# Performance work log

Hardware: AMD Instinct MI355X
Metric: run time of the kernel (lower is better)

Reference implementation:

```python
import jax, jax.numpy as jnp
import numpy as np

B, S, IN, E, H, NH = 32, 1024, 16, 128, 256, 4
DH = E // NH
EPS = 1e-5


def _ln(x, g, b):
    mu = jnp.mean(x, axis=-1, keepdims=True)
    var = jnp.mean(jnp.square(x - mu), axis=-1, keepdims=True)
    return (x - mu) * jax.lax.rsqrt(var + EPS) * g + b


def setup_inputs() -> dict:
    key = jax.random.key(0)
    ks = iter(jax.random.split(key, 32))
    n = lambda shape, s=0.02: jax.random.normal(next(ks), shape, jnp.float32) * s
    inp = {
        "x": jax.random.normal(next(ks), (B, S, IN), jnp.float32),
        "mask": jax.random.uniform(next(ks), (B, S), jnp.float32),
        "embed_w": n((E, IN)), "embed_b": jnp.zeros((E,), jnp.float32),
        # 3 encoder layers, params stacked on leading layer axis
        "in_proj_w": n((3, 3 * E, E)), "in_proj_b": jnp.zeros((3, 3 * E), jnp.float32),
        "out_w": n((3, E, E)), "out_b": jnp.zeros((3, E), jnp.float32),
        "ln1_g": jnp.ones((3, E), jnp.float32), "ln1_b": jnp.zeros((3, E), jnp.float32),
        "ln2_g": jnp.ones((3, E), jnp.float32), "ln2_b": jnp.zeros((3, E), jnp.float32),
        "ffn_w1": n((3, E, E)), "ffn_b1": jnp.zeros((3, E), jnp.float32),
        "ffn_w2": n((3, E, E)), "ffn_b2": jnp.zeros((3, E), jnp.float32),
        "cls_w1": n((H, E)), "cls_b1": jnp.zeros((H,), jnp.float32),
        "cls_w2": n((H, H)), "cls_b2": jnp.zeros((H,), jnp.float32),
        "cls_w3": n((H, H)), "cls_b3": jnp.zeros((H,), jnp.float32),
        "cls_w4": n((1, H)), "cls_b4": jnp.zeros((1,), jnp.float32),
    }
    return inp


def _encoder_layer(x, ipw, ipb, ow, ob, g1, b1, g2, b2, w1, fb1, w2, fb2):
    # PyTorch TransformerEncoderLayer, norm_first=False (post-norm), relu FFN
    qkv = x @ ipw.T + ipb                      # [B,S,3E]
    q, k, v = jnp.split(qkv, 3, axis=-1)
    q = q.reshape(B, S, NH, DH).transpose(0, 2, 1, 3)
    k = k.reshape(B, S, NH, DH).transpose(0, 2, 1, 3)
    v = v.reshape(B, S, NH, DH).transpose(0, 2, 1, 3)
    scores = jnp.einsum("bhqd,bhkd->bhqk", q, k) / np.sqrt(DH)  # naive O(S^2) math SDPA
    attn = jax.nn.softmax(scores, axis=-1)
    o = jnp.einsum("bhqk,bhkd->bhqd", attn, v)
    o = o.transpose(0, 2, 1, 3).reshape(B, S, E) @ ow.T + ob
    x = _ln(x + o, g1, b1)
    ff = jax.nn.relu(x @ w1.T + fb1) @ w2.T + fb2
    return _ln(x + ff, g2, b2)


def reference(x, mask, embed_w, embed_b, in_proj_w, in_proj_b, out_w, out_b,
              ln1_g, ln1_b, ln2_g, ln2_b, ffn_w1, ffn_b1, ffn_w2, ffn_b2,
              cls_w1, cls_b1, cls_w2, cls_b2, cls_w3, cls_b3, cls_w4, cls_b4):
    h = jax.nn.relu(x @ embed_w.T + embed_b)   # [B,S,E]
    for i in range(3):
        h = _encoder_layer(h, in_proj_w[i], in_proj_b[i], out_w[i], out_b[i],
                           ln1_g[i], ln1_b[i], ln2_g[i], ln2_b[i],
                           ffn_w1[i], ffn_b1[i], ffn_w2[i], ffn_b2[i])
    pooled = jnp.sum(h * mask[:, :, None], axis=1)  # [B,E] masked sum pool
    z = jax.nn.relu(pooled @ cls_w1.T + cls_b1)
    z = jax.nn.relu(z @ cls_w2.T + cls_b2)
    z = jax.nn.relu(z @ cls_w3.T + cls_b3)
    return jax.nn.sigmoid(z @ cls_w4.T + cls_b4)    # [B,1]
```

## Files before the change

kernel.cpp:

```cpp
#include <hip/hip_runtime.h>
#include <hip/hip_bf16.h>
#include <math.h>

#define B 32
#define S 1024
#define IN_DIM 16
#define E 128
#define NH 4
#define DH 32
#define HDIM 256
#define ROWS (B*S)
#define EPS 1e-5f

#define N_IPW (3*384*128)
#define N_SQ  (3*128*128)
#define NCVT ((N_IPW + 3*N_SQ) / 256)

typedef __bf16 bf16x8 __attribute__((ext_vector_type(8)));
typedef __bf16 bf16x4 __attribute__((ext_vector_type(4)));
typedef __bf16 bf16x2 __attribute__((ext_vector_type(2)));
typedef float f32x4 __attribute__((ext_vector_type(4)));
typedef float f32x16 __attribute__((ext_vector_type(16)));

#define MFMA16 __builtin_amdgcn_mfma_f32_16x16x32_bf16
#define MFMA32 __builtin_amdgcn_mfma_f32_32x32x16_bf16

union BF2U { bf16x2 b; unsigned int u; };
__device__ inline unsigned int pk2(float a, float b) {
    BF2U x; x.b[0] = (__bf16)a; x.b[1] = (__bf16)b; return x.u;
}

union U8 { bf16x8 v8; bf16x4 v4[2]; unsigned u4[4]; };
__device__ inline void st8(__bf16* p, bf16x8 v) {
    U8 u; u.v8 = v;
    *(bf16x4*)p = u.v4[0];
    *(bf16x4*)(p + 4) = u.v4[1];
}
__device__ inline bf16x8 ld8(const __bf16* p) {
    U8 u;
    u.v4[0] = *(const bf16x4*)p;
    u.v4[1] = *(const bf16x4*)(p + 4);
    return u.v8;
}

__global__ __launch_bounds__(256) void k_embedcvt(
        const float* __restrict__ ipw, const float* __restrict__ ow,
        const float* __restrict__ w1, const float* __restrict__ w2,
        __bf16* __restrict__ wbo,
        const float* __restrict__ x, const float* __restrict__ W,
        const float* __restrict__ bias, __bf16* __restrict__ hb)
{
    int t = threadIdx.x;
    if (blockIdx.x < NCVT) {
        int i = blockIdx.x * 256 + t;
        float v;
        if (i < N_IPW) v = ipw[i];
        else if (i < N_IPW + N_SQ) v = ow[i - N_IPW];
        else if (i < N_IPW + 2 * N_SQ) v = w1[i - N_IPW - N_SQ];
        else v = w2[i - N_IPW - 2 * N_SQ];
        wbo[i] = (__bf16)v;
        return;
    }
    int row0 = (blockIdx.x - NCVT) * 16;
    __shared__ float xs[16][16];
    xs[t >> 4][t & 15] = x[(row0 + (t >> 4)) * IN_DIM + (t & 15)];
    __syncthreads();
    int sub = t >> 7, tc = t & 127;
    float w[16];
#pragma unroll
    for (int i = 0; i < 16; ++i) w[i] = W[tc * 16 + i];
    float bb = bias[tc];
#pragma unroll
    for (int rr = 0; rr < 8; ++rr) {
        int lr = sub * 8 + rr;
        float acc = bb;
#pragma unroll
        for (int i = 0; i < 16; ++i) acc += xs[lr][i] * w[i];
        hb[(size_t)(row0 + lr) * E + tc] = (__bf16)fmaxf(acc, 0.f);
    }
}

__global__ __launch_bounds__(1024, 4) void k_qkvattn(
        const __bf16* __restrict__ hb, const __bf16* __restrict__ Wip,
        const float* __restrict__ bip, __bf16* __restrict__ O)
{
    __shared__ __attribute__((aligned(16))) __bf16 Ksh[1024][36];
    __shared__ __attribute__((aligned(16))) __bf16 Vsh[32][1036];
    __shared__ float lscr[16][32];

    int t = threadIdx.x, lane = t & 63, wv = t >> 6;
    int l15 = lane & 15, quad = lane >> 4;
    int l31 = lane & 31, hi = lane >> 5;
    int lb = ((blockIdx.x & 7) << 5) | (blockIdx.x >> 3);
    int half = lb & 1, bh = lb >> 1;
    int hh = bh & 3, b = bh >> 2;

    const __bf16* hpanel = hb + (size_t)b * S * E;

    const float qscale = 0.1767766952966369f * 1.4426950408889634f * 8388608.0f;
    const float C2 = 1065101558.0f;
    f32x16 cinit16, z16;
#pragma unroll
    for (int i = 0; i < 16; ++i) { cinit16[i] = C2; z16[i] = 0.f; }

    bf16x8 bQ[2];
    {
        bf16x8 bWq[8];
#pragma unroll
        for (int ch = 0; ch < 8; ++ch)
            bWq[ch] = *(const bf16x8*)&Wip[(size_t)(hh*32 + l31)*128 + ch*16 + hi*8];
        float bq = bip[hh*32 + l31];
        int qrow0 = half*512 + wv*32;
        f32x16 aq = z16;
#pragma unroll
        for (int ch = 0; ch < 8; ++ch) {
            bf16x8 ah = *(const bf16x8*)&hpanel[(size_t)(qrow0 + l31)*128 + ch*16 + hi*8];
            aq = MFMA32(ah, bWq[ch], aq, 0, 0, 0);
        }
        __bf16* PmS = &Ksh[wv*32][0];
#pragma unroll
        for (int r = 0; r < 16; ++r) {
            int q = (r & 3) + 8*(r >> 2) + 4*hi;
            PmS[q*36 + l31] = (__bf16)((aq[r] + bq) * qscale);
        }
        __asm__ __volatile__("" ::: "memory");
        bQ[0] = ld8(&PmS[l31*36 + hi*8]);
        bQ[1] = ld8(&PmS[l31*36 + 16 + hi*8]);
        __asm__ __volatile__("" ::: "memory");
    }
    __syncthreads();

    {
        bf16x8 bWk[2][4], bWv[2][4];
#pragma unroll
        for (int df = 0; df < 2; ++df)
#pragma unroll
            for (int kc = 0; kc < 4; ++kc) {
                bWk[df][kc] = *(const bf16x8*)&Wip[(size_t)(128 + hh*32 + df*16 + l15)*128 + kc*32 + quad*8];
                bWv[df][kc] = *(const bf16x8*)&Wip[(size_t)(256 + hh*32 + df*16 + l15)*128 + kc*32 + quad*8];
            }
        float bk0 = bip[128 + hh*32 + l15],  bk1 = bip[128 + hh*32 + 16 + l15];
        float bvb0 = bip[256 + hh*32 + l15], bvb1 = bip[256 + hh*32 + 16 + l15];
        int srow = wv*16 + l15;
        bf16x8 af[4], ag[4];
#pragma unroll
        for (int kc = 0; kc < 4; ++kc)
            af[kc] = *(const bf16x8*)&hpanel[(size_t)srow*128 + kc*32 + quad*8];
        const f32x4 z4 = {0.f, 0.f, 0.f, 0.f};
        for (int c = 0; c < 4; ++c) {
            if (c < 3) {
#pragma unroll
                for (int kc = 0; kc < 4; ++kc)
                    ag[kc] = *(const bf16x8*)&hpanel[(size_t)((c+1)*256 + srow)*128 + kc*32 + quad*8];
            }
            f32x4 k0 = z4, k1 = z4, v0 = z4, v1 = z4;
#pragma unroll
            for (int kc = 0; kc < 4; ++kc) {
                k0 = MFMA16(af[kc], bWk[0][kc], k0, 0, 0, 0);
                k1 = MFMA16(af[kc], bWk[1][kc], k1, 0, 0, 0);
                v0 = MFMA16(af[kc], bWv[0][kc], v0, 0, 0, 0);
                v1 = MFMA16(af[kc], bWv[1][kc], v1, 0, 0, 0);
            }
            int s0 = c*256 + wv*16 + quad*4;
#pragma unroll
            for (int r = 0; r < 4; ++r) {
                Ksh[s0 + r][l15]      = (__bf16)(k0[r] + bk0);
                Ksh[s0 + r][16 + l15] = (__bf16)(k1[r] + bk1);
            }
            uint2 u0, u1;
            u0.x = pk2(v0[0] + bvb0, v0[1] + bvb0);
            u0.y = pk2(v0[2] + bvb0, v0[3] + bvb0);
            u1.x = pk2(v1[0] + bvb1, v1[1] + bvb1);
            u1.y = pk2(v1[2] + bvb1, v1[3] + bvb1);
            *(uint2*)&Vsh[l15][s0] = u0;
            *(uint2*)&Vsh[16 + l15][s0] = u1;
#pragma unroll
            for (int kc = 0; kc < 4; ++kc) af[kc] = ag[kc];
        }
    }
    __syncthreads();

    f32x16 o = z16;
    float lsum = 0.f;

    for (int c = 0; c < 16; ++c) {
        bf16x8 aK[2][2];
#pragma unroll
        for (int sub = 0; sub < 2; ++sub)
#pragma unroll
            for (int dh = 0; dh < 2; ++dh)
                aK[sub][dh] = ld8(&Ksh[c*64 + sub*32 + l31][dh*16 + hi*8]);
        bf16x8 bVf[4];
#pragma unroll
        for (int ch = 0; ch < 4; ++ch) {
            U8 u;
            const __bf16* vp = &Vsh[l31][c*64 + ch*16 + hi*4];
            u.v4[0] = *(const bf16x4*)vp;
            u.v4[1] = *(const bf16x4*)(vp + 8);
            bVf[ch] = u.v8;
        }
#pragma unroll
        for (int sub = 0; sub < 2; ++sub) {
            f32x16 acc = cinit16;
            acc = MFMA32(aK[sub][0], bQ[0], acc, 0, 0, 0);
            acc = MFMA32(aK[sub][1], bQ[1], acc, 0, 0, 0);
#pragma unroll
            for (int g = 0; g < 2; ++g) {
                U8 u;
#pragma unroll
                for (int r = 0; r < 4; ++r) {
                    int ia = (int)acc[g*8 + 2*r];
                    int ib = (int)acc[g*8 + 2*r + 1];
                    u.u4[r] = __builtin_amdgcn_perm((unsigned)ib, (unsigned)ia, 0x07060302u);
                    lsum += __int_as_float(ia) + __int_as_float(ib);
                }
                o = MFMA32(u.v8, bVf[sub*2 + g], o, 0, 0, 0);
            }
        }
    }

    lsum += __shfl_xor(lsum, 32);
    float linv = 1.f / lsum;
    if (hi == 0) lscr[wv][l31] = linv;
    __asm__ __volatile__("" ::: "memory");
#pragma unroll
    for (int r = 0; r < 16; ++r) {
        int q = (r & 3) + 8*(r >> 2) + 4*hi;
        float li = lscr[wv][q];
        int row = half*512 + wv*32 + q;
        O[((size_t)(b * S) + row) * E + hh*32 + l31] = (__bf16)(o[r] * li);
    }
}

__global__ __launch_bounds__(512, 4) void k_layer2(const __bf16* __restrict__ t0b,
        const __bf16* __restrict__ Wo, const float* __restrict__ ob,
        const float* __restrict__ g1, const float* __restrict__ bt1,
        const __bf16* __restrict__ W1, const float* __restrict__ b1v,
        const __bf16* __restrict__ W2, const float* __restrict__ b2v,
        const float* __restrict__ g2, const float* __restrict__ bt2,
        __bf16* __restrict__ hb)
{
    __shared__ __attribute__((aligned(16))) __bf16 As[64][132];
    __shared__ __attribute__((aligned(16))) __bf16 Ws[128][132];
    __shared__ float red[2][64][2];
    int t = threadIdx.x;
    int m0 = blockIdx.x * 64;
    int arow = t >> 3, acol = (t & 7) * 16;
    int wrow = t >> 2, wcol = (t & 3) * 32;
    {
        const __bf16* Ap = t0b + (size_t)(m0 + arow) * 128 + acol;
#pragma unroll
        for (int j = 0; j < 2; ++j)
            st8(&As[arow][acol + j * 8], *(const bf16x8*)&Ap[j * 8]);
        const __bf16* Wp = Wo + (size_t)wrow * 128 + wcol;
#pragma unroll
        for (int j = 0; j < 4; ++j)
            st8(&Ws[wrow][wcol + j * 8], *(const bf16x8*)&Wp[j * 8]);
    }
    __syncthreads();
    int lane = t & 63, wv = t >> 6;
    int l15 = lane & 15, quad = lane >> 4;
    int nh = wv & 1, mh = wv >> 1;
    f32x4 acc[4];

#pragma unroll
    for (int i = 0; i < 4; ++i) acc[i] = (f32x4){0.f, 0.f, 0.f, 0.f};
#pragma unroll
    for (int kc = 0; kc < 4; ++kc) {
        bf16x8 aw[4], ba;
#pragma unroll
        for (int nc = 0; nc < 4; ++nc)
            aw[nc] = ld8(&Ws[nh * 64 + nc * 16 + l15][kc * 32 + quad * 8]);
        ba = ld8(&As[mh * 16 + l15][kc * 32 + quad * 8]);
#pragma unroll
        for (int nc = 0; nc < 4; ++nc)
            acc[nc] = MFMA16(aw[nc], ba, acc[nc], 0, 0, 0);
    }
    float s1 = 0.f, s2 = 0.f;
    int m = m0 + mh * 16 + l15;
#pragma unroll
    for (int nc = 0; nc < 4; ++nc) {
        float4 bv = *(const float4*)&ob[nh * 64 + nc * 16 + quad * 4];
        bf16x4 rv = *(const bf16x4*)&hb[(size_t)m * 128 + nh * 64 + nc * 16 + quad * 4];
        acc[nc][0] += bv.x + (float)rv[0];
        acc[nc][1] += bv.y + (float)rv[1];
        acc[nc][2] += bv.z + (float)rv[2];
        acc[nc][3] += bv.w + (float)rv[3];
#pragma unroll
        for (int i = 0; i < 4; ++i) {
            s1 += acc[nc][i];
            s2 += acc[nc][i] * acc[nc][i];
        }
    }
    s1 += __shfl_xor(s1, 16); s1 += __shfl_xor(s1, 32);
    s2 += __shfl_xor(s2, 16); s2 += __shfl_xor(s2, 32);
    if (quad == 0) {
        red[nh][mh * 16 + l15][0] = s1;
        red[nh][mh * 16 + l15][1] = s2;
    }
    __syncthreads();
    float mu, rs;
    {
        int r = mh * 16 + l15;
        float S1 = red[0][r][0] + red[1][r][0];
        float S2 = red[0][r][1] + red[1][r][1];
        mu = S1 * (1.f / 128.f);
        float var = S2 * (1.f / 128.f) - mu * mu;
        rs = rsqrtf(var + EPS);
    }
    bf16x4 res2[4];
#pragma unroll
    for (int nc = 0; nc < 4; ++nc) {
        float4 gv = *(const float4*)&g1[nh * 64 + nc * 16 + quad * 4];
        float4 bb = *(const float4*)&bt1[nh * 64 + nc * 16 + quad * 4];
        float o0 = (acc[nc][0] - mu) * rs * gv.x + bb.x;
        float o1 = (acc[nc][1] - mu) * rs * gv.y + bb.y;
        float o2 = (acc[nc][2] - mu) * rs * gv.z + bb.z;
        float o3 = (acc[nc][3] - mu) * rs * gv.w + bb.w;
        bf16x4 xb;
        xb[0] = (__bf16)o0; xb[1] = (__bf16)o1;
        xb[2] = (__bf16)o2; xb[3] = (__bf16)o3;
        res2[nc] = xb;
        *(bf16x4*)&As[mh * 16 + l15][nh * 64 + nc * 16 + quad * 4] = xb;
    }
    {
        const __bf16* Wp = W1 + (size_t)wrow * 128 + wcol;
#pragma unroll
        for (int j = 0; j < 4; ++j)
            st8(&Ws[wrow][wcol + j * 8], *(const bf16x8*)&Wp[j * 8]);
    }
    __syncthreads();

#pragma unroll
    for (int i = 0; i < 4; ++i) acc[i] = (f32x4){0.f, 0.f, 0.f, 0.f};
#pragma unroll
    for (int kc = 0; kc < 4; ++kc) {
        bf16x8 aw[4], ba;
#pragma unroll
        for (int nc = 0; nc < 4; ++nc)
            aw[nc] = ld8(&Ws[nh * 64 + nc * 16 + l15][kc * 32 + quad * 8]);
        ba = ld8(&As[mh * 16 + l15][kc * 32 + quad * 8]);
#pragma unroll
        for (int nc = 0; nc < 4; ++nc)
            acc[nc] = MFMA16(aw[nc], ba, acc[nc], 0, 0, 0);
    }
    __syncthreads();
#pragma unroll
    for (int nc = 0; nc < 4; ++nc) {
        float4 bv = *(const float4*)&b1v[nh * 64 + nc * 16 + quad * 4];
        float v0 = fmaxf(acc[nc][0] + bv.x, 0.f);
        float v1 = fmaxf(acc[nc][1] + bv.y, 0.f);
        float v2 = fmaxf(acc[nc][2] + bv.z, 0.f);
        float v3 = fmaxf(acc[nc][3] + bv.w, 0.f);
        uint2 u; u.x = pk2(v0, v1); u.y = pk2(v2, v3);
        *(uint2*)&As[mh * 16 + l15][nh * 64 + nc * 16 + quad * 4] = u;
    }
    {
        const __bf16* Wp = W2 + (size_t)wrow * 128 + wcol;
#pragma unroll
        for (int j = 0; j < 4; ++j)
            st8(&Ws[wrow][wcol + j * 8], *(const bf16x8*)&Wp[j * 8]);
    }
    __syncthreads();

#pragma unroll
    for (int i = 0; i < 4; ++i) acc[i] = (f32x4){0.f, 0.f, 0.f, 0.f};
#pragma unroll
    for (int kc = 0; kc < 4; ++kc) {
        bf16x8 aw[4], ba;
#pragma unroll
        for (int nc = 0; nc < 4; ++nc)
            aw[nc] = ld8(&Ws[nh * 64 + nc * 16 + l15][kc * 32 + quad * 8]);
        ba = ld8(&As[mh * 16 + l15][kc * 32 + quad * 8]);
#pragma unroll
        for (int nc = 0; nc < 4; ++nc)
            acc[nc] = MFMA16(aw[nc], ba, acc[nc], 0, 0, 0);
    }
    s1 = 0.f; s2 = 0.f;
#pragma unroll
    for (int nc = 0; nc < 4; ++nc) {
        float4 bv = *(const float4*)&b2v[nh * 64 + nc * 16 + quad * 4];
        acc[nc][0] += bv.x + (float)res2[nc][0];
        acc[nc][1] += bv.y + (float)res2[nc][1];
        acc[nc][2] += bv.z + (float)res2[nc][2];
        acc[nc][3] += bv.w + (float)res2[nc][3];
#pragma unroll
        for (int i = 0; i < 4; ++i) {
            s1 += acc[nc][i];
            s2 += acc[nc][i] * acc[nc][i];
        }
    }
    s1 += __shfl_xor(s1, 16); s1 += __shfl_xor(s1, 32);
    s2 += __shfl_xor(s2, 16); s2 += __shfl_xor(s2, 32);
    if (quad == 0) {
        red[nh][mh * 16 + l15][0] = s1;
        red[nh][mh * 16 + l15][1] = s2;
    }
    __syncthreads();
    {
        int r = mh * 16 + l15;
        float S1 = red[0][r][0] + red[1][r][0];
        float S2 = red[0][r][1] + red[1][r][1];
        mu = S1 * (1.f / 128.f);
        float var = S2 * (1.f / 128.f) - mu * mu;
        rs = rsqrtf(var + EPS);
    }
#pragma unroll
    for (int nc = 0; nc < 4; ++nc) {
        float4 gv = *(const float4*)&g2[nh * 64 + nc * 16 + quad * 4];
        float4 bb = *(const float4*)&bt2[nh * 64 + nc * 16 + quad * 4];
        float o0 = (acc[nc][0] - mu) * rs * gv.x + bb.x;
        float o1 = (acc[nc][1] - mu) * rs * gv.y + bb.y;
        float o2 = (acc[nc][2] - mu) * rs * gv.z + bb.z;
        float o3 = (acc[nc][3] - mu) * rs * gv.w + bb.w;
        uint2 u; u.x = pk2(o0, o1); u.y = pk2(o2, o3);
        *(uint2*)&hb[(size_t)m * 128 + nh * 64 + nc * 16 + quad * 4] = u;
    }
}

__global__ __launch_bounds__(256) void k_pool1(const __bf16* __restrict__ h,
        const float* __restrict__ mask, float* __restrict__ part)
{
    int bx = blockIdx.x;
    int b = bx >> 3, ch = bx & 7, t = threadIdx.x;
    int sg = t >> 4, cg = t & 15;
    __shared__ float red[16][128];
    float acc[8];
#pragma unroll
    for (int j = 0; j < 8; ++j) acc[j] = 0.f;
    const __bf16* hp = h + ((size_t)(b * S + ch * 128 + sg)) * E + cg * 8;
    const float* mp = mask + b * S + ch * 128 + sg;
#pragma unroll
    for (int k = 0; k < 8; ++k) {
        float m = mp[k * 16];
        bf16x8 hv = *(const bf16x8*)&hp[(size_t)(k * 16) * E];
#pragma unroll
        for (int j = 0; j < 8; ++j) acc[j] += (float)hv[j] * m;
    }
#pragma unroll
    for (int j = 0; j < 8; ++j) red[sg][cg * 8 + j] = acc[j];
    __syncthreads();
    if (t < 128) {
        float a = 0.f;
#pragma unroll
        for (int sgi = 0; sgi < 16; ++sgi) a += red[sgi][t];
        part[(size_t)bx * E + t] = a;
    }
}

__global__ __launch_bounds__(256) void k_head(const float* __restrict__ part,
        const float* __restrict__ cw1, const float* __restrict__ cb1,
        const float* __restrict__ cw2, const float* __restrict__ cb2,
        const float* __restrict__ cw3, const float* __restrict__ cb3,
        const float* __restrict__ cw4, const float* __restrict__ cb4,
        float* __restrict__ out)
{
    int b = blockIdx.x, t = threadIdx.x;
    __shared__ float p[128], za[256], zb[256];
    __shared__ float red4[4];
    if (t < 128) {
        float a = 0.f;
#pragma unroll
        for (int c = 0; c < 8; ++c) a += part[(size_t)(b * 8 + c) * 128 + t];
        p[t] = a;
    }
    __syncthreads();
    float a1 = cb1[t];
    for (int k = 0; k < 128; ++k) a1 += p[k] * cw1[t * 128 + k];
    za[t] = fmaxf(a1, 0.f);
    __syncthreads();
    float a2 = cb2[t];
    for (int k = 0; k < 256; ++k) a2 += za[k] * cw2[t * 256 + k];
    zb[t] = fmaxf(a2, 0.f);
    __syncthreads();
    float a3 = cb3[t];
    for (int k = 0; k < 256; ++k) a3 += zb[k] * cw3[t * 256 + k];
    float z3 = fmaxf(a3, 0.f);
    float prt = z3 * cw4[t];
#pragma unroll
    for (int o2 = 32; o2; o2 >>= 1) prt += __shfl_xor(prt, o2);
    if ((t & 63) == 0) red4[t >> 6] = prt;
    __syncthreads();
    if (t == 0) {
        float sum = red4[0] + red4[1] + red4[2] + red4[3] + cb4[0];
        out[b] = 1.f / (1.f + __expf(-sum));
    }
}

extern "C" void kernel_launch(void* const* d_in, const int* in_sizes, int n_in,
                              void* d_out, int out_size, void* d_ws, size_t ws_size,
                              hipStream_t stream)
{
    const float* x     = (const float*)d_in[0];
    const float* mask  = (const float*)d_in[1];
    const float* emb_w = (const float*)d_in[2];
    const float* emb_b = (const float*)d_in[3];
    const float* ipw   = (const float*)d_in[4];
    const float* ipb   = (const float*)d_in[5];
    const float* ow    = (const float*)d_in[6];
    const float* ob    = (const float*)d_in[7];
    const float* ln1g  = (const float*)d_in[8];
    const float* ln1b  = (const float*)d_in[9];
    const float* ln2g  = (const float*)d_in[10];
    const float* ln2b  = (const float*)d_in[11];
    const float* w1    = (const float*)d_in[12];
    const float* fb1   = (const float*)d_in[13];
    const float* w2    = (const float*)d_in[14];
    const float* fb2   = (const float*)d_in[15];
    const float* cw1   = (const float*)d_in[16];
    const float* cb1   = (const float*)d_in[17];
    const float* cw2   = (const float*)d_in[18];
    const float* cb2   = (const float*)d_in[19];
    const float* cw3   = (const float*)d_in[20];
    const float* cb3   = (const float*)d_in[21];
    const float* cw4   = (const float*)d_in[22];
    const float* cb4   = (const float*)d_in[23];

    char* p = (char*)d_ws;
    __bf16* hb   = (__bf16*)p;   p += (size_t)ROWS * E * 2;
    p += (size_t)ROWS * 256 * 2;
    p += (size_t)ROWS * 32 * 4 * 2 / 4;
    __bf16* t0b  = (__bf16*)p;   p += (size_t)ROWS * E * 2;
    __bf16* wb   = (__bf16*)p;   p += (size_t)(N_IPW + 3 * N_SQ) * 2;
    float* part  = (float*)p;    p += (size_t)B * 8 * E * 4;

    __bf16* wb_ipw = wb;
    __bf16* wb_ow  = wb + N_IPW;
    __bf16* wb_w1  = wb_ow + N_SQ;
    __bf16* wb_w2  = wb_w1 + N_SQ;

    k_embedcvt<<<NCVT + ROWS / 16, 256, 0, stream>>>(
        ipw, ow, w1, w2, wb, x, emb_w, emb_b, hb);
    for (int L = 0; L < 3; ++L) {
        k_qkvattn<<<B * NH * 2, 1024, 0, stream>>>(
            hb, wb_ipw + (size_t)L * 384 * 128, ipb + L * 384, t0b);
        k_layer2<<<ROWS / 64, 512, 0, stream>>>(
            t0b, wb_ow + (size_t)L * 128 * 128, ob + L * 128,
            ln1g + L * E, ln1b + L * E,
            wb_w1 + (size_t)L * 128 * 128, fb1 + L * 128,
            wb_w2 + (size_t)L * 128 * 128, fb2 + L * 128,
            ln2g + L * E, ln2b + L * E, hb);
    }
    k_pool1<<<B * 8, 256, 0, stream>>>(hb, mask, part);
    k_head<<<B, 256, 0, stream>>>(part, cw1, cb1, cw2, cb2, cw3, cb3, cw4, cb4,
                                  (float*)d_out);
}
```

Baseline: 306.5 us.

## Give each attention wave two query tiles, software-pipeline K/V loads, prefetch layer2 weights

The attention kernel now runs with 512 threads per block, and each wave handles two 32-row query tiles. Each K/V fragment loaded from shared memory is reused across both tiles, and the next chunk's K/V fragments are loaded while the current chunk computes. The layer2 kernel issues its global loads for the residual and the W1/W2 weights early into registers, so that global latency overlaps compute; its launch-bounds occupancy hint drops to 3. This trades higher register pressure and fewer waves per block for less LDS traffic and less exposed latency.

```diff
diff --git a/kernel.cpp b/kernel.cpp
--- a/kernel.cpp
+++ b/kernel.cpp
@@ -80,13 +80,13 @@
     }
 }
 
-__global__ __launch_bounds__(1024, 4) void k_qkvattn(
+__global__ __launch_bounds__(512, 2) void k_qkvattn(
         const __bf16* __restrict__ hb, const __bf16* __restrict__ Wip,
         const float* __restrict__ bip, __bf16* __restrict__ O)
 {
     __shared__ __attribute__((aligned(16))) __bf16 Ksh[1024][36];
     __shared__ __attribute__((aligned(16))) __bf16 Vsh[32][1036];
-    __shared__ float lscr[16][32];
+    __shared__ float lscr[8][64];
 
     int t = threadIdx.x, lane = t & 63, wv = t >> 6;
     int l15 = lane & 15, quad = lane >> 4;
@@ -103,29 +103,36 @@
 #pragma unroll
     for (int i = 0; i < 16; ++i) { cinit16[i] = C2; z16[i] = 0.f; }
 
-    bf16x8 bQ[2];
+    bf16x8 bQ[2][2];
     {
         bf16x8 bWq[8];
 #pragma unroll
         for (int ch = 0; ch < 8; ++ch)
             bWq[ch] = *(const bf16x8*)&Wip[(size_t)(hh*32 + l31)*128 + ch*16 + hi*8];
         float bq = bip[hh*32 + l31];
-        int qrow0 = half*512 + wv*32;
-        f32x16 aq = z16;
-#pragma unroll
-        for (int ch = 0; ch < 8; ++ch) {
-            bf16x8 ah = *(const bf16x8*)&hpanel[(size_t)(qrow0 + l31)*128 + ch*16 + hi*8];
-            aq = MFMA32(ah, bWq[ch], aq, 0, 0, 0);
-        }
-        __bf16* PmS = &Ksh[wv*32][0];
-#pragma unroll
-        for (int r = 0; r < 16; ++r) {
-            int q = (r & 3) + 8*(r >> 2) + 4*hi;
-            PmS[q*36 + l31] = (__bf16)((aq[r] + bq) * qscale);
+#pragma unroll
+        for (int qt = 0; qt < 2; ++qt) {
+            int qrow0 = half*512 + wv*64 + qt*32;
+            f32x16 aq = z16;
+#pragma unroll
+            for (int ch = 0; ch < 8; ++ch) {
+                bf16x8 ah = *(const bf16x8*)&hpanel[(size_t)(qrow0 + l31)*128 + ch*16 + hi*8];
+                aq = MFMA32(ah, bWq[ch], aq, 0, 0, 0);
+            }
+            __bf16* PmS = &Ksh[wv*128 + qt*32][0];
+#pragma unroll
+            for (int r = 0; r < 16; ++r) {
+                int q = (r & 3) + 8*(r >> 2) + 4*hi;
+                PmS[q*36 + l31] = (__bf16)((aq[r] + bq) * qscale);
+            }
         }
         __asm__ __volatile__("" ::: "memory");
-        bQ[0] = ld8(&PmS[l31*36 + hi*8]);
-        bQ[1] = ld8(&PmS[l31*36 + 16 + hi*8]);
+#pragma unroll
+        for (int qt = 0; qt < 2; ++qt) {
+            const __bf16* PmS = &Ksh[wv*128 + qt*32][0];
+            bQ[qt][0] = ld8(&PmS[l31*36 + hi*8]);
+            bQ[qt][1] = ld8(&PmS[l31*36 + 16 + hi*8]);
+        }
         __asm__ __volatile__("" ::: "memory");
     }
     __syncthreads();
@@ -147,11 +154,11 @@
         for (int kc = 0; kc < 4; ++kc)
             af[kc] = *(const bf16x8*)&hpanel[(size_t)srow*128 + kc*32 + quad*8];
         const f32x4 z4 = {0.f, 0.f, 0.f, 0.f};
-        for (int c = 0; c < 4; ++c) {
-            if (c < 3) {
+        for (int c = 0; c < 8; ++c) {
+            if (c < 7) {
 #pragma unroll
                 for (int kc = 0; kc < 4; ++kc)
-                    ag[kc] = *(const bf16x8*)&hpanel[(size_t)((c+1)*256 + srow)*128 + kc*32 + quad*8];
+                    ag[kc] = *(const bf16x8*)&hpanel[(size_t)((c+1)*128 + srow)*128 + kc*32 + quad*8];
             }
             f32x4 k0 = z4, k1 = z4, v0 = z4, v1 = z4;
 #pragma unroll
@@ -161,7 +168,7 @@
                 v0 = MFMA16(af[kc], bWv[0][kc], v0, 0, 0, 0);
                 v1 = MFMA16(af[kc], bWv[1][kc], v1, 0, 0, 0);
             }
-            int s0 = c*256 + wv*16 + quad*4;
+            int s0 = c*128 + wv*16 + quad*4;
 #pragma unroll
             for (int r = 0; r < 4; ++r) {
                 Ksh[s0 + r][l15]      = (__bf16)(k0[r] + bk0);
@@ -180,59 +187,94 @@
     }
     __syncthreads();
 
-    f32x16 o = z16;
-    float lsum = 0.f;
+    f32x16 o[2];
+    o[0] = z16; o[1] = z16;
+    float lsum[2] = {0.f, 0.f};
+
+    bf16x8 aK[2][2], bVf[4];
+#pragma unroll
+    for (int sub = 0; sub < 2; ++sub)
+#pragma unroll
+        for (int dh = 0; dh < 2; ++dh)
+            aK[sub][dh] = ld8(&Ksh[sub*32 + l31][dh*16 + hi*8]);
+#pragma unroll
+    for (int ch = 0; ch < 4; ++ch) {
+        U8 u;
+        const __bf16* vp = &Vsh[l31][ch*16 + hi*4];
+        u.v4[0] = *(const bf16x4*)vp;
+        u.v4[1] = *(const bf16x4*)(vp + 8);
+        bVf[ch] = u.v8;
+    }
 
     for (int c = 0; c < 16; ++c) {
-        bf16x8 aK[2][2];
-#pragma unroll
-        for (int sub = 0; sub < 2; ++sub)
-#pragma unroll
-            for (int dh = 0; dh < 2; ++dh)
-                aK[sub][dh] = ld8(&Ksh[c*64 + sub*32 + l31][dh*16 + hi*8]);
-        bf16x8 bVf[4];
-#pragma unroll
-        for (int ch = 0; ch < 4; ++ch) {
-            U8 u;
-            const __bf16* vp = &Vsh[l31][c*64 + ch*16 + hi*4];
-            u.v4[0] = *(const bf16x4*)vp;
-            u.v4[1] = *(const bf16x4*)(vp + 8);
-            bVf[ch] = u.v8;
-        }
-#pragma unroll
-        for (int sub = 0; sub < 2; ++sub) {
-            f32x16 acc = cinit16;
-            acc = MFMA32(aK[sub][0], bQ[0], acc, 0, 0, 0);
-            acc = MFMA32(aK[sub][1], bQ[1], acc, 0, 0, 0);
-#pragma unroll
-            for (int g = 0; g < 2; ++g) {
+        bf16x8 aKn[2][2], bVn[4];
+        if (c < 15) {
+#pragma unroll
+            for (int sub = 0; sub < 2; ++sub)
+#pragma unroll
+                for (int dh = 0; dh < 2; ++dh)
+                    aKn[sub][dh] = ld8(&Ksh[(c+1)*64 + sub*32 + l31][dh*16 + hi*8]);
+#pragma unroll
+            for (int ch = 0; ch < 4; ++ch) {
                 U8 u;
-#pragma unroll
-                for (int r = 0; r < 4; ++r) {
-                    int ia = (int)acc[g*8 + 2*r];
-                    int ib = (int)acc[g*8 + 2*r + 1];
-                    u.u4[r] = __builtin_amdgcn_perm((unsigned)ib, (unsigned)ia, 0x07060302u);
-                    lsum += __int_as_float(ia) + __int_as_float(ib);
+                const __bf16* vp = &Vsh[l31][(c+1)*64 + ch*16 + hi*4];
+                u.v4[0] = *(const bf16x4*)vp;
+                u.v4[1] = *(const bf16x4*)(vp + 8);
+                bVn[ch] = u.v8;
+            }
+        }
+#pragma unroll
+        for (int qt = 0; qt < 2; ++qt) {
+#pragma unroll
+            for (int sub = 0; sub < 2; ++sub) {
+                f32x16 acc = cinit16;
+                acc = MFMA32(aK[sub][0], bQ[qt][0], acc, 0, 0, 0);
+                acc = MFMA32(aK[sub][1], bQ[qt][1], acc, 0, 0, 0);
+#pragma unroll
+                for (int g = 0; g < 2; ++g) {
+                    U8 u;
+                    float ls = 0.f;
+#pragma unroll
+                    for (int r = 0; r < 4; ++r) {
+                        int ia = (int)acc[g*8 + 2*r];
+                        int ib = (int)acc[g*8 + 2*r + 1];
+                        u.u4[r] = __builtin_amdgcn_perm((unsigned)ib, (unsigned)ia, 0x07060302u);
+                        ls += __int_as_float(ia) + __int_as_float(ib);
+                    }
+                    lsum[qt] += ls;
+                    o[qt] = MFMA32(u.v8, bVf[sub*2 + g], o[qt], 0, 0, 0);
                 }
-                o = MFMA32(u.v8, bVf[sub*2 + g], o, 0, 0, 0);
-            }
-        }
-    }
-
-    lsum += __shfl_xor(lsum, 32);
-    float linv = 1.f / lsum;
-    if (hi == 0) lscr[wv][l31] = linv;
+            }
+        }
+        if (c < 15) {
+#pragma unroll
+            for (int sub = 0; sub < 2; ++sub)
+#pragma unroll
+                for (int dh = 0; dh < 2; ++dh)
+                    aK[sub][dh] = aKn[sub][dh];
+#pragma unroll
+            for (int ch = 0; ch < 4; ++ch) bVf[ch] = bVn[ch];
+        }
+    }
+
+#pragma unroll
+    for (int qt = 0; qt < 2; ++qt) {
+        float ls = lsum[qt] + __shfl_xor(lsum[qt], 32);
+        if (hi == 0) lscr[wv][qt*32 + l31] = 1.f / ls;
+    }
     __asm__ __volatile__("" ::: "memory");
 #pragma unroll
-    for (int r = 0; r < 16; ++r) {
-        int q = (r & 3) + 8*(r >> 2) + 4*hi;
-        float li = lscr[wv][q];
-        int row = half*512 + wv*32 + q;
-        O[((size_t)(b * S) + row) * E + hh*32 + l31] = (__bf16)(o[r] * li);
-    }
-}
-
-__global__ __launch_bounds__(512, 4) void k_layer2(const __bf16* __restrict__ t0b,
+    for (int qt = 0; qt < 2; ++qt)
+#pragma unroll
+        for (int r = 0; r < 16; ++r) {
+            int q = (r & 3) + 8*(r >> 2) + 4*hi;
+            float li = lscr[wv][qt*32 + q];
+            int row = half*512 + wv*64 + qt*32 + q;
+            O[((size_t)(b * S) + row) * E + hh*32 + l31] = (__bf16)(o[qt][r] * li);
+        }
+}
+
+__global__ __launch_bounds__(512, 3) void k_layer2(const __bf16* __restrict__ t0b,
         const __bf16* __restrict__ Wo, const float* __restrict__ ob,
         const float* __restrict__ g1, const float* __restrict__ bt1,
         const __bf16* __restrict__ W1, const float* __restrict__ b1v,
@@ -245,22 +287,36 @@
     __shared__ float red[2][64][2];
     int t = threadIdx.x;
     int m0 = blockIdx.x * 64;
-    int arow = t >> 3, acol = (t & 7) * 16;
-    int wrow = t >> 2, wcol = (t & 3) * 32;
-    {
-        const __bf16* Ap = t0b + (size_t)(m0 + arow) * 128 + acol;
-#pragma unroll
-        for (int j = 0; j < 2; ++j)
-            st8(&As[arow][acol + j * 8], *(const bf16x8*)&Ap[j * 8]);
-        const __bf16* Wp = Wo + (size_t)wrow * 128 + wcol;
-#pragma unroll
-        for (int j = 0; j < 4; ++j)
-            st8(&Ws[wrow][wcol + j * 8], *(const bf16x8*)&Wp[j * 8]);
-    }
-    __syncthreads();
     int lane = t & 63, wv = t >> 6;
     int l15 = lane & 15, quad = lane >> 4;
     int nh = wv & 1, mh = wv >> 1;
+    int m = m0 + mh * 16 + l15;
+    int arow = t >> 3, acol = (t & 7) * 16;
+    int wrow = t >> 2, wcol = (t & 3) * 32;
+
+    bf16x8 avr[2], w0r[4], w1r[4];
+    {
+        const __bf16* Ap = t0b + (size_t)(m0 + arow) * 128 + acol;
+        avr[0] = *(const bf16x8*)&Ap[0];
+        avr[1] = *(const bf16x8*)&Ap[8];
+        const __bf16* Wp0 = Wo + (size_t)wrow * 128 + wcol;
+        const __bf16* Wp1 = W1 + (size_t)wrow * 128 + wcol;
+#pragma unroll
+        for (int j = 0; j < 4; ++j) w0r[j] = *(const bf16x8*)&Wp0[j * 8];
+#pragma unroll
+        for (int j = 0; j < 4; ++j) w1r[j] = *(const bf16x8*)&Wp1[j * 8];
+    }
+    bf16x4 rv[4];
+#pragma unroll
+    for (int nc = 0; nc < 4; ++nc)
+        rv[nc] = *(const bf16x4*)&hb[(size_t)m * 128 + nh * 64 + nc * 16 + quad * 4];
+
+#pragma unroll
+    for (int j = 0; j < 2; ++j) st8(&As[arow][acol + j * 8], avr[j]);
+#pragma unroll
+    for (int j = 0; j < 4; ++j) st8(&Ws[wrow][wcol + j * 8], w0r[j]);
+    __syncthreads();
+
     f32x4 acc[4];
 
 #pragma unroll
@@ -277,15 +333,13 @@
             acc[nc] = MFMA16(aw[nc], ba, acc[nc], 0, 0, 0);
     }
     float s1 = 0.f, s2 = 0.f;
-    int m = m0 + mh * 16 + l15;
 #pragma unroll
     for (int nc = 0; nc < 4; ++nc) {
         float4 bv = *(const float4*)&ob[nh * 64 + nc * 16 + quad * 4];
-        bf16x4 rv = *(const bf16x4*)&hb[(size_t)m * 128 + nh * 64 + nc * 16 + quad * 4];
-        acc[nc][0] += bv.x + (float)rv[0];
-        acc[nc][1] += bv.y + (float)rv[1];
-        acc[nc][2] += bv.z + (float)rv[2];
-        acc[nc][3] += bv.w + (float)rv[3];
+        acc[nc][0] += bv.x + (float)rv[nc][0];
+        acc[nc][1] += bv.y + (float)rv[nc][1];
+        acc[nc][2] += bv.z + (float)rv[nc][2];
+        acc[nc][3] += bv.w + (float)rv[nc][3];
 #pragma unroll
         for (int i = 0; i < 4; ++i) {
             s1 += acc[nc][i];
@@ -299,6 +353,14 @@
         red[nh][mh * 16 + l15][1] = s2;
     }
     __syncthreads();
+#pragma unroll
+    for (int j = 0; j < 4; ++j) st8(&Ws[wrow][wcol + j * 8], w1r[j]);
+    bf16x8 w2r[4];
+    {
+        const __bf16* Wp2 = W2 + (size_t)wrow * 128 + wcol;
+#pragma unroll
+        for (int j = 0; j < 4; ++j) w2r[j] = *(const bf16x8*)&Wp2[j * 8];
+    }
     float mu, rs;
     {
         int r = mh * 16 + l15;
@@ -323,12 +385,6 @@
         res2[nc] = xb;
         *(bf16x4*)&As[mh * 16 + l15][nh * 64 + nc * 16 + quad * 4] = xb;
     }
-    {
-        const __bf16* Wp = W1 + (size_t)wrow * 128 + wcol;
-#pragma unroll
-        for (int j = 0; j < 4; ++j)
-            st8(&Ws[wrow][wcol + j * 8], *(const bf16x8*)&Wp[j * 8]);
-    }
     __syncthreads();
 
 #pragma unroll
@@ -355,12 +411,8 @@
         uint2 u; u.x = pk2(v0, v1); u.y = pk2(v2, v3);
         *(uint2*)&As[mh * 16 + l15][nh * 64 + nc * 16 + quad * 4] = u;
     }
-    {
-        const __bf16* Wp = W2 + (size_t)wrow * 128 + wcol;
-#pragma unroll
-        for (int j = 0; j < 4; ++j)
-            st8(&Ws[wrow][wcol + j * 8], *(const bf16x8*)&Wp[j * 8]);
-    }
+#pragma unroll
+    for (int j = 0; j < 4; ++j) st8(&Ws[wrow][wcol + j * 8], w2r[j]);
     __syncthreads();
 
 #pragma unroll
@@ -532,7 +584,7 @@
     k_embedcvt<<<NCVT + ROWS / 16, 256, 0, stream>>>(
         ipw, ow, w1, w2, wb, x, emb_w, emb_b, hb);
     for (int L = 0; L < 3; ++L) {
-        k_qkvattn<<<B * NH * 2, 1024, 0, stream>>>(
+        k_qkvattn<<<B * NH * 2, 512, 0, stream>>>(
             hb, wb_ipw + (size_t)L * 384 * 128, ipb + L * 384, t0b);
         k_layer2<<<ROWS / 64, 512, 0, stream>>>(
             t0b, wb_ow + (size_t)L * 128 * 128, ob + L * 128,
```

Measured after the change: 302.0 us. About the same (-1.5%).
